# Optimization experiments

Hardware: AMD Instinct MI355X
Metric: run time of the kernel (lower is better)

Reference implementation:

```python
import jax, jax.numpy as jnp
import numpy as np

N_NODES = 50000
N_EDGES = 800000
HIDDEN = 128


def setup_inputs() -> dict:
    key = jax.random.key(0)
    ks = jax.random.split(key, 8)
    z = jax.random.normal(ks[0], (N_NODES, HIDDEN), dtype=jnp.float32)
    weights = jax.random.normal(ks[1], (N_EDGES, 1), dtype=jnp.float32)
    sources = jax.random.randint(ks[2], (N_EDGES,), 0, N_NODES)
    dests = jax.random.randint(ks[3], (N_EDGES,), 0, N_NODES)
    # Linear params (stored [in, out]); scale ~ 1/sqrt(fan_in) like torch default
    in_m = 2 * HIDDEN + 1
    in_u = 2 * HIDDEN
    Wm = jax.random.uniform(ks[4], (in_m, HIDDEN), dtype=jnp.float32, minval=-1.0, maxval=1.0) / np.sqrt(in_m)
    bm = jax.random.uniform(ks[5], (HIDDEN,), dtype=jnp.float32, minval=-1.0, maxval=1.0) / np.sqrt(in_m)
    Wu = jax.random.uniform(ks[6], (in_u, HIDDEN), dtype=jnp.float32, minval=-1.0, maxval=1.0) / np.sqrt(in_u)
    bu = jax.random.uniform(ks[7], (HIDDEN,), dtype=jnp.float32, minval=-1.0, maxval=1.0) / np.sqrt(in_u)
    return {"z": z, "weights": weights, "sources": sources, "dests": dests,
            "Wm": Wm, "bm": bm, "Wu": Wu, "bu": bu}


def reference(z, weights, sources, dests, Wm, bm, Wu, bu):
    n = z.shape[0]
    # gather + concat message input: [E, 2d+1]
    inp = jnp.concatenate([z[dests], z[sources], weights], axis=1)
    messages = inp @ Wm + bm                      # [E, d]
    # scatter_reduce amax over destination nodes; empty segments -> -inf
    m = jax.ops.segment_max(messages, dests, num_segments=n)
    m = jnp.where(jnp.isneginf(m), jnp.zeros_like(m), m)
    h = jnp.concatenate([z, m], axis=1) @ Wu + bu  # [N, d]
    return h
```

## Files before the change

kernel.cpp:

```cpp
#include <hip/hip_runtime.h>
#include <math.h>

#define HIDDEN 128
#define PAD_DEG 64
#define NPART 8
#define CHUNK 2048

typedef __attribute__((ext_vector_type(8))) _Float16 f16x8;
typedef __attribute__((ext_vector_type(4))) float f32x4;
typedef __attribute__((ext_vector_type(2))) _Float16 h2;

__device__ inline unsigned short f2h(float x) {
    _Float16 h = (_Float16)x;
    return __builtin_bit_cast(unsigned short, h);
}
__device__ inline float h2f(unsigned short u) {
    return (float)__builtin_bit_cast(_Float16, u);
}
__device__ inline float h2f_lo(unsigned int u) { return h2f((unsigned short)(u & 0xffff)); }
__device__ inline float h2f_hi(unsigned int u) { return h2f((unsigned short)(u >> 16)); }
__device__ inline h2 hmax2(h2 a, h2 b) {
    h2 r;
    r[0] = a[0] > b[0] ? a[0] : b[0];
    r[1] = a[1] > b[1] ? a[1] : b[1];
    return r;
}

__global__ void prep_kernel(const float* __restrict__ Wm, const float* __restrict__ Wu,
                            unsigned short* __restrict__ WmT0, unsigned short* __restrict__ WmT1,
                            unsigned short* __restrict__ WuT, float* __restrict__ wlast,
                            int* __restrict__ counts, int n) {
    int t = blockIdx.x * blockDim.x + threadIdx.x;
    if (t < 16384) {
        int nn = t >> 7, k = t & 127;
        WmT0[t] = f2h(Wm[k * 128 + nn]);
    } else if (t < 32768) {
        int s = t - 16384;
        int nn = s >> 7, k = s & 127;
        WmT1[s] = f2h(Wm[(128 + k) * 128 + nn]);
    } else if (t < 65536) {
        int s = t - 32768;
        int nn = s >> 8, k = s & 255;
        WuT[s] = f2h(Wu[k * 128 + nn]);
    } else if (t < 65664) {
        int i = t - 65536;
        wlast[i] = Wm[256 * 128 + i];
    } else if (t < 65664 + n) {
        counts[t - 65664] = 0;
    }
}

__global__ __launch_bounds__(256) void gemm_msg(const float* __restrict__ Z,
                                                const unsigned short* __restrict__ WmT0,
                                                const unsigned short* __restrict__ WmT1,
                                                unsigned short* __restrict__ P1h,
                                                unsigned short* __restrict__ P2h,
                                                int n) {
    __shared__ unsigned short As[64][136];
    __shared__ unsigned short Bs[128][136];

    const int m0 = blockIdx.x * 64;
    const int tid = threadIdx.x;
    const int wave = tid >> 6, lane = tid & 63;
    const int l15 = lane & 15, q = lane >> 4;
    const int wrow = wave * 16;

#pragma unroll
    for (int i = 0; i < 4; ++i) {
        int f = tid + i * 256;
        int row = f >> 4, c8 = f & 15;
        int gr = min(m0 + row, n - 1);
        const float4* src = (const float4*)&Z[(size_t)gr * 128 + c8 * 8];
        float4 a = src[0], b = src[1];
        f16x8 hv;
        hv[0] = (_Float16)a.x; hv[1] = (_Float16)a.y; hv[2] = (_Float16)a.z; hv[3] = (_Float16)a.w;
        hv[4] = (_Float16)b.x; hv[5] = (_Float16)b.y; hv[6] = (_Float16)b.z; hv[7] = (_Float16)b.w;
        *(f16x8*)&As[row][c8 * 8] = hv;
    }

    for (int part = 0; part < 2; ++part) {
        const float4* bsrc = (const float4*)(part == 0 ? WmT0 : WmT1);
        unsigned short* Out = part == 0 ? P1h : P2h;

#pragma unroll
        for (int i = 0; i < 8; ++i) {
            int f = tid + i * 256;
            int row = f >> 4, c4 = f & 15;
            *(float4*)&Bs[row][c4 * 8] = bsrc[row * 16 + c4];
        }
        __syncthreads();

        f32x4 acc[8];
#pragma unroll
        for (int nt = 0; nt < 8; ++nt) acc[nt] = (f32x4){0.f, 0.f, 0.f, 0.f};

#pragma unroll
        for (int ks = 0; ks < 4; ++ks) {
            int k0 = ks * 32;
            f16x8 a = *(const f16x8*)&As[wrow + l15][k0 + q * 8];
#pragma unroll
            for (int nt = 0; nt < 8; ++nt) {
                f16x8 b = *(const f16x8*)&Bs[nt * 16 + l15][k0 + q * 8];
                acc[nt] = __builtin_amdgcn_mfma_f32_16x16x32_f16(a, b, acc[nt], 0, 0, 0);
            }
        }

#pragma unroll
        for (int nt = 0; nt < 8; ++nt) {
#pragma unroll
            for (int r = 0; r < 4; ++r) {
                int row = m0 + wrow + q * 4 + r;
                if (row < n) Out[(size_t)row * 128 + nt * 16 + l15] = f2h(acc[nt][r]);
            }
        }
        __syncthreads();
    }
}

__global__ __launch_bounds__(256) void scatter_part(const int* __restrict__ dests,
                                                    const int* __restrict__ sources,
                                                    const float* __restrict__ weights,
                                                    int* __restrict__ counts,
                                                    unsigned int* __restrict__ edge_pk,
                                                    int E, int span, int n) {
    const int part = blockIdx.x & (NPART - 1);
    const int chunk = blockIdx.x >> 3;
    const int lo = part * span;
    const int hi = min(lo + span, n);
    const int base = chunk * CHUNK;

#pragma unroll
    for (int i = 0; i < CHUNK; i += 256) {
        int e = base + i + threadIdx.x;
        if (e < E) {
            int d = dests[e];
            if (d >= lo && d < hi) {
                int pos = atomicAdd(&counts[d], 1);
                if (pos < PAD_DEG) {
                    unsigned int pk = (unsigned int)(sources[e] & 0xffff) |
                                      ((unsigned int)f2h(weights[e]) << 16);
                    edge_pk[(size_t)d * PAD_DEG + pos] = pk;
                }
            }
        }
    }
}

__global__ __launch_bounds__(256) void segmax_kernel(const unsigned short* __restrict__ P1h,
                                                     const unsigned short* __restrict__ P2h,
                                                     const int* __restrict__ counts,
                                                     const unsigned int* __restrict__ edge_pk,
                                                     const float* __restrict__ wlast,
                                                     const float* __restrict__ bm,
                                                     unsigned short* __restrict__ Mh, int n) {
    const int wave = threadIdx.x >> 6;
    const int lane = threadIdx.x & 63;
    const int v = blockIdx.x * 4 + wave;
    if (v >= n) return;

    const int l32 = lane & 31;
    const int half = lane >> 5;
    const uint2* P2q = (const uint2*)P2h;
    const int cnt = min(counts[v], PAD_DEG);

    int pk = (lane < cnt) ? (int)edge_pk[(size_t)v * PAD_DEG + lane] : 0;

    float4 wl4 = ((const float4*)wlast)[l32];
    h2 wlv0; wlv0[0] = (_Float16)wl4.x; wlv0[1] = (_Float16)wl4.y;
    h2 wlv1; wlv1[0] = (_Float16)wl4.z; wlv1[1] = (_Float16)wl4.w;

    const h2 NEGINF = __builtin_bit_cast(h2, 0xFC00FC00u);
    h2 acc0 = NEGINF, acc1 = NEGINF;

    int j = 0;
    for (; j + 4 <= cnt; j += 4) {
        unsigned int pa = (unsigned int)__shfl(pk, j + half);
        unsigned int pb = (unsigned int)__shfl(pk, j + 2 + half);
        {
            int src = pa & 0xffff;
            unsigned int wd = (pa & 0xffff0000u) | (pa >> 16);
            h2 wv = __builtin_bit_cast(h2, wd);
            uint2 u = P2q[(size_t)src * 32 + l32];
            acc0 = hmax2(acc0, wv * wlv0 + __builtin_bit_cast(h2, u.x));
            acc1 = hmax2(acc1, wv * wlv1 + __builtin_bit_cast(h2, u.y));
        }
        {
            int src = pb & 0xffff;
            unsigned int wd = (pb & 0xffff0000u) | (pb >> 16);
            h2 wv = __builtin_bit_cast(h2, wd);
            uint2 u = P2q[(size_t)src * 32 + l32];
            acc0 = hmax2(acc0, wv * wlv0 + __builtin_bit_cast(h2, u.x));
            acc1 = hmax2(acc1, wv * wlv1 + __builtin_bit_cast(h2, u.y));
        }
    }
    for (; j + 2 <= cnt; j += 2) {
        unsigned int pa = (unsigned int)__shfl(pk, j + half);
        int src = pa & 0xffff;
        unsigned int wd = (pa & 0xffff0000u) | (pa >> 16);
        h2 wv = __builtin_bit_cast(h2, wd);
        uint2 u = P2q[(size_t)src * 32 + l32];
        acc0 = hmax2(acc0, wv * wlv0 + __builtin_bit_cast(h2, u.x));
        acc1 = hmax2(acc1, wv * wlv1 + __builtin_bit_cast(h2, u.y));
    }
    if (j < cnt) {
        unsigned int pa = (unsigned int)__shfl(pk, j);
        if (half == 0) {
            int src = pa & 0xffff;
            unsigned int wd = (pa & 0xffff0000u) | (pa >> 16);
            h2 wv = __builtin_bit_cast(h2, wd);
            uint2 u = P2q[(size_t)src * 32 + l32];
            acc0 = hmax2(acc0, wv * wlv0 + __builtin_bit_cast(h2, u.x));
            acc1 = hmax2(acc1, wv * wlv1 + __builtin_bit_cast(h2, u.y));
        }
    }

    acc0 = hmax2(acc0, __builtin_bit_cast(h2, __shfl_xor(__builtin_bit_cast(int, acc0), 32)));
    acc1 = hmax2(acc1, __builtin_bit_cast(h2, __shfl_xor(__builtin_bit_cast(int, acc1), 32)));

    if (half == 0) {
        float m0 = 0.f, m1 = 0.f, m2 = 0.f, m3 = 0.f;
        if (cnt > 0) {
            uint2 p1v = ((const uint2*)P1h)[(size_t)v * 32 + l32];
            float4 b4 = ((const float4*)bm)[l32];
            m0 = h2f_lo(p1v.x) + b4.x + (float)acc0[0];
            m1 = h2f_hi(p1v.x) + b4.y + (float)acc0[1];
            m2 = h2f_lo(p1v.y) + b4.z + (float)acc1[0];
            m3 = h2f_hi(p1v.y) + b4.w + (float)acc1[1];
        }
        uint2 o;
        o.x = (unsigned int)f2h(m0) | ((unsigned int)f2h(m1) << 16);
        o.y = (unsigned int)f2h(m2) | ((unsigned int)f2h(m3) << 16);
        ((uint2*)Mh)[(size_t)v * 32 + l32] = o;
    }
}

__global__ __launch_bounds__(256) void gemm_out(const float* __restrict__ Z,
                                                const unsigned short* __restrict__ Mh,
                                                const unsigned short* __restrict__ WuT,
                                                const float* __restrict__ bu,
                                                float* __restrict__ H, int n) {
    __shared__ unsigned short As[64][136];
    __shared__ unsigned short Bs[128][136];

    const int m0 = blockIdx.x * 64;
    const int tid = threadIdx.x;
    const int wave = tid >> 6, lane = tid & 63;
    const int l15 = lane & 15, q = lane >> 4;
    const int wrow = wave * 16;

    f32x4 acc[8];
#pragma unroll
    for (int nt = 0; nt < 8; ++nt) acc[nt] = (f32x4){0.f, 0.f, 0.f, 0.f};

    for (int h = 0; h < 2; ++h) {
#pragma unroll
        for (int i = 0; i < 8; ++i) {
            int f = tid + i * 256;
            int row = f >> 4, c4 = f & 15;
            *(float4*)&Bs[row][c4 * 8] = ((const float4*)WuT)[row * 32 + h * 16 + c4];
        }
        if (h == 0) {
#pragma unroll
            for (int i = 0; i < 4; ++i) {
                int f = tid + i * 256;
                int row = f >> 4, c8 = f & 15;
                int gr = min(m0 + row, n - 1);
                const float4* src = (const float4*)&Z[(size_t)gr * 128 + c8 * 8];
                float4 a = src[0], b = src[1];
                f16x8 hv;
                hv[0] = (_Float16)a.x; hv[1] = (_Float16)a.y; hv[2] = (_Float16)a.z; hv[3] = (_Float16)a.w;
                hv[4] = (_Float16)b.x; hv[5] = (_Float16)b.y; hv[6] = (_Float16)b.z; hv[7] = (_Float16)b.w;
                *(f16x8*)&As[row][c8 * 8] = hv;
            }
        } else {
#pragma unroll
            for (int i = 0; i < 4; ++i) {
                int f = tid + i * 256;
                int row = f >> 4, c4 = f & 15;
                int gr = min(m0 + row, n - 1);
                *(float4*)&As[row][c4 * 8] = ((const float4*)&Mh[(size_t)gr * 128])[c4];
            }
        }
        __syncthreads();

#pragma unroll
        for (int ks = 0; ks < 4; ++ks) {
            int k0 = ks * 32;
            f16x8 a = *(const f16x8*)&As[wrow + l15][k0 + q * 8];
#pragma unroll
            for (int nt = 0; nt < 8; ++nt) {
                f16x8 b = *(const f16x8*)&Bs[nt * 16 + l15][k0 + q * 8];
                acc[nt] = __builtin_amdgcn_mfma_f32_16x16x32_f16(a, b, acc[nt], 0, 0, 0);
            }
        }
        __syncthreads();
    }

#pragma unroll
    for (int nt = 0; nt < 8; ++nt) {
        int col = nt * 16 + l15;
        float bias = bu[col];
#pragma unroll
        for (int r = 0; r < 4; ++r) {
            int row = m0 + wrow + q * 4 + r;
            if (row < n) H[(size_t)row * 128 + col] = acc[nt][r] + bias;
        }
    }
}

extern "C" void kernel_launch(void* const* d_in, const int* in_sizes, int n_in,
                              void* d_out, int out_size, void* d_ws, size_t ws_size,
                              hipStream_t stream) {
    const float* z = (const float*)d_in[0];
    const float* weights = (const float*)d_in[1];
    const int* sources = (const int*)d_in[2];
    const int* dests = (const int*)d_in[3];
    const float* Wm = (const float*)d_in[4];
    const float* bm = (const float*)d_in[5];
    const float* Wu = (const float*)d_in[6];
    const float* bu = (const float*)d_in[7];

    const int n = in_sizes[0] / HIDDEN;
    const int E = in_sizes[1];
    float* H = (float*)d_out;

    char* w = (char*)d_ws;
    auto alloc = [&](size_t bytes) { void* p = w; w += (bytes + 255) & ~(size_t)255; return p; };
    unsigned short* P1h = (unsigned short*)alloc((size_t)n * 128 * 2);
    unsigned short* Mh  = (unsigned short*)alloc((size_t)n * 128 * 2);
    unsigned short* WmT0 = (unsigned short*)alloc(16384 * 2);
    unsigned short* WmT1 = (unsigned short*)alloc(16384 * 2);
    unsigned short* WuT  = (unsigned short*)alloc(32768 * 2);
    float* wlast = (float*)alloc(128 * 4);
    int* counts  = (int*)alloc((size_t)n * 4);
    unsigned int* edge_pk = (unsigned int*)alloc((size_t)n * PAD_DEG * 4);

    unsigned short* P2h = (unsigned short*)d_out;

    const int mblocks = (n + 63) / 64;
    const int prep_threads = 65664 + n;
    const int span = (n + NPART - 1) / NPART;
    const int nchunks = (E + CHUNK - 1) / CHUNK;

    prep_kernel<<<(prep_threads + 255) / 256, 256, 0, stream>>>(Wm, Wu, WmT0, WmT1, WuT,
                                                                wlast, counts, n);
    gemm_msg<<<mblocks, 256, 0, stream>>>(z, WmT0, WmT1, P1h, P2h, n);
    scatter_part<<<nchunks * NPART, 256, 0, stream>>>(dests, sources, weights, counts,
                                                      edge_pk, E, span, n);
    segmax_kernel<<<(n + 3) / 4, 256, 0, stream>>>(P1h, P2h, counts, edge_pk,
                                                   wlast, bm, Mh, n);
    gemm_out<<<mblocks, 256, 0, stream>>>(z, Mh, WuT, bu, H, n);
}
```

Before: 192.7 us.

## Replace partition-filtered edge scatter with two-pass binning through staging buckets

The old scatter kernel read every edge once per destination partition (8 passes) and filtered by range. Now a binning kernel reads each edge once and uses wave ballots with one atomic per wave per partition to append packed (dest, source|weight) entries into 64 staging buckets. A placement kernel, with blocks interleaved by partition, then does the per-node atomic slot assignment into the padded adjacency. This trades the repeated edge reads for an extra launch and a staging write and read-back. Buckets are capped at a fixed capacity, so skewed destination distributions could silently drop edges.

```diff
diff --git a/kernel.cpp b/kernel.cpp
--- a/kernel.cpp
+++ b/kernel.cpp
@@ -5,6 +5,8 @@
 #define PAD_DEG 64
 #define NPART 8
 #define CHUNK 2048
+#define CAP 16384
+#define PB_J 48
 
 typedef __attribute__((ext_vector_type(8))) _Float16 f16x8;
 typedef __attribute__((ext_vector_type(4))) float f32x4;
@@ -29,7 +31,7 @@
 __global__ void prep_kernel(const float* __restrict__ Wm, const float* __restrict__ Wu,
                             unsigned short* __restrict__ WmT0, unsigned short* __restrict__ WmT1,
                             unsigned short* __restrict__ WuT, float* __restrict__ wlast,
-                            int* __restrict__ counts, int n) {
+                            int* __restrict__ counts, int* __restrict__ pcur, int n) {
     int t = blockIdx.x * blockDim.x + threadIdx.x;
     if (t < 16384) {
         int nn = t >> 7, k = t & 127;
@@ -47,6 +49,8 @@
         wlast[i] = Wm[256 * 128 + i];
     } else if (t < 65664 + n) {
         counts[t - 65664] = 0;
+    } else if (t < 65664 + n + 64) {
+        pcur[t - 65664 - n] = 0;
     }
 }
 
@@ -117,31 +121,62 @@
     }
 }
 
-__global__ __launch_bounds__(256) void scatter_part(const int* __restrict__ dests,
-                                                    const int* __restrict__ sources,
-                                                    const float* __restrict__ weights,
-                                                    int* __restrict__ counts,
-                                                    unsigned int* __restrict__ edge_pk,
-                                                    int E, int span, int n) {
-    const int part = blockIdx.x & (NPART - 1);
-    const int chunk = blockIdx.x >> 3;
-    const int lo = part * span;
-    const int hi = min(lo + span, n);
-    const int base = chunk * CHUNK;
+__global__ __launch_bounds__(256) void bin_kernel(const int* __restrict__ dests,
+                                                  const int* __restrict__ sources,
+                                                  const float* __restrict__ weights,
+                                                  int* __restrict__ pcur,
+                                                  uint2* __restrict__ staging,
+                                                  int E, int span) {
+    const int myb = blockIdx.x & 7;
+    const int base = blockIdx.x * CHUNK;
+    const int lane = threadIdx.x & 63;
 
 #pragma unroll
     for (int i = 0; i < CHUNK; i += 256) {
         int e = base + i + threadIdx.x;
-        if (e < E) {
-            int d = dests[e];
-            if (d >= lo && d < hi) {
-                int pos = atomicAdd(&counts[d], 1);
-                if (pos < PAD_DEG) {
-                    unsigned int pk = (unsigned int)(sources[e] & 0xffff) |
-                                      ((unsigned int)f2h(weights[e]) << 16);
-                    edge_pk[(size_t)d * PAD_DEG + pos] = pk;
-                }
-            }
+        bool valid = e < E;
+        int d = 0;
+        unsigned int pk = 0;
+        if (valid) {
+            d = dests[e];
+            pk = (unsigned int)(sources[e] & 0xffff) |
+                 ((unsigned int)f2h(weights[e]) << 16);
+        }
+        int p = valid ? (d / span) : -1;
+#pragma unroll
+        for (int pp = 0; pp < NPART; ++pp) {
+            unsigned long long m = __ballot(p == pp);
+            if (m == 0ull) continue;
+            int leader = __ffsll((long long)m) - 1;
+            int cnt = __popcll(m);
+            int rbase = 0;
+            if (lane == leader) rbase = atomicAdd(&pcur[pp * 8 + myb], cnt);
+            rbase = __shfl(rbase, leader);
+            if (p == pp) {
+                int off = __popcll(m & ((1ull << lane) - 1ull));
+                int idx = rbase + off;
+                if (idx < CAP)
+                    staging[(size_t)(pp * 8 + myb) * CAP + idx] = make_uint2((unsigned)d, pk);
+            }
+        }
+    }
+}
+
+__global__ __launch_bounds__(256) void place_kernel(const int* __restrict__ pcur,
+                                                    const uint2* __restrict__ staging,
+                                                    int* __restrict__ counts,
+                                                    unsigned int* __restrict__ edge_pk) {
+    const int p = blockIdx.x & 7;
+    const int j = blockIdx.x >> 3;
+
+    for (int r = 0; r < 8; ++r) {
+        int total = min(pcur[p * 8 + r], CAP);
+        const uint2* reg = staging + (size_t)(p * 8 + r) * CAP;
+        for (int i = j * 256 + threadIdx.x; i < total; i += PB_J * 256) {
+            uint2 ent = reg[i];
+            int d = (int)ent.x;
+            int pos = atomicAdd(&counts[d], 1);
+            if (pos < PAD_DEG) edge_pk[(size_t)d * PAD_DEG + pos] = ent.y;
         }
     }
 }
@@ -333,20 +368,22 @@
     unsigned short* WuT  = (unsigned short*)alloc(32768 * 2);
     float* wlast = (float*)alloc(128 * 4);
     int* counts  = (int*)alloc((size_t)n * 4);
+    int* pcur    = (int*)alloc(64 * 4);
     unsigned int* edge_pk = (unsigned int*)alloc((size_t)n * PAD_DEG * 4);
+    uint2* staging = (uint2*)alloc((size_t)64 * CAP * 8);
 
     unsigned short* P2h = (unsigned short*)d_out;
 
     const int mblocks = (n + 63) / 64;
-    const int prep_threads = 65664 + n;
+    const int prep_threads = 65664 + n + 64;
     const int span = (n + NPART - 1) / NPART;
     const int nchunks = (E + CHUNK - 1) / CHUNK;
 
     prep_kernel<<<(prep_threads + 255) / 256, 256, 0, stream>>>(Wm, Wu, WmT0, WmT1, WuT,
-                                                                wlast, counts, n);
+                                                                wlast, counts, pcur, n);
     gemm_msg<<<mblocks, 256, 0, stream>>>(z, WmT0, WmT1, P1h, P2h, n);
-    scatter_part<<<nchunks * NPART, 256, 0, stream>>>(dests, sources, weights, counts,
-                                                      edge_pk, E, span, n);
+    bin_kernel<<<nchunks, 256, 0, stream>>>(dests, sources, weights, pcur, staging, E, span);
+    place_kernel<<<NPART * PB_J, 256, 0, stream>>>(pcur, staging, counts, edge_pk);
     segmax_kernel<<<(n + 3) / 4, 256, 0, stream>>>(P1h, P2h, counts, edge_pk,
                                                    wlast, bm, Mh, n);
     gemm_out<<<mblocks, 256, 0, stream>>>(z, Mh, WuT, bu, H, n);
```

Result: slower. 707.5 us (+267.1%).

## Fuse message GEMM with edge scatter and drop LDS staging in GEMMs

Applied to the files above, without the earlier changes.

Merges the message GEMM and the edge-bucketing scatter into one launch: the first blocks do the GEMM and the remaining blocks do the scatter. This removes one launch and lets the compute-bound and atomic-bound work overlap on the GPU. Both GEMM kernels also stop staging A and B tiles in shared memory and stop calling __syncthreads. Each lane now loads its MFMA fragments straight from global memory (Z, Mh and the transposed weights), relying on cache hits for the reused weight tiles. The risk is more global and L2 traffic, and less coalesced fragment loads, in exchange for no LDS use and no barriers.

```diff
diff --git a/kernel.cpp b/kernel.cpp
--- a/kernel.cpp
+++ b/kernel.cpp
@@ -50,96 +50,81 @@
     }
 }
 
-__global__ __launch_bounds__(256) void gemm_msg(const float* __restrict__ Z,
-                                                const unsigned short* __restrict__ WmT0,
-                                                const unsigned short* __restrict__ WmT1,
-                                                unsigned short* __restrict__ P1h,
-                                                unsigned short* __restrict__ P2h,
-                                                int n) {
-    __shared__ unsigned short As[64][136];
-    __shared__ unsigned short Bs[128][136];
-
-    const int m0 = blockIdx.x * 64;
+__global__ __launch_bounds__(256) void fused_msg_scatter(
+        const float* __restrict__ Z,
+        const unsigned short* __restrict__ WmT0,
+        const unsigned short* __restrict__ WmT1,
+        unsigned short* __restrict__ P1h,
+        unsigned short* __restrict__ P2h,
+        const int* __restrict__ dests,
+        const int* __restrict__ sources,
+        const float* __restrict__ weights,
+        int* __restrict__ counts,
+        unsigned int* __restrict__ edge_pk,
+        int n, int E, int span, int mblocks) {
     const int tid = threadIdx.x;
-    const int wave = tid >> 6, lane = tid & 63;
-    const int l15 = lane & 15, q = lane >> 4;
-    const int wrow = wave * 16;
-
-#pragma unroll
-    for (int i = 0; i < 4; ++i) {
-        int f = tid + i * 256;
-        int row = f >> 4, c8 = f & 15;
-        int gr = min(m0 + row, n - 1);
-        const float4* src = (const float4*)&Z[(size_t)gr * 128 + c8 * 8];
-        float4 a = src[0], b = src[1];
-        f16x8 hv;
-        hv[0] = (_Float16)a.x; hv[1] = (_Float16)a.y; hv[2] = (_Float16)a.z; hv[3] = (_Float16)a.w;
-        hv[4] = (_Float16)b.x; hv[5] = (_Float16)b.y; hv[6] = (_Float16)b.z; hv[7] = (_Float16)b.w;
-        *(f16x8*)&As[row][c8 * 8] = hv;
-    }
-
-    for (int part = 0; part < 2; ++part) {
-        const float4* bsrc = (const float4*)(part == 0 ? WmT0 : WmT1);
-        unsigned short* Out = part == 0 ? P1h : P2h;
-
-#pragma unroll
-        for (int i = 0; i < 8; ++i) {
-            int f = tid + i * 256;
-            int row = f >> 4, c4 = f & 15;
-            *(float4*)&Bs[row][c4 * 8] = bsrc[row * 16 + c4];
-        }
-        __syncthreads();
-
-        f32x4 acc[8];
-#pragma unroll
-        for (int nt = 0; nt < 8; ++nt) acc[nt] = (f32x4){0.f, 0.f, 0.f, 0.f};
-
-#pragma unroll
-        for (int ks = 0; ks < 4; ++ks) {
-            int k0 = ks * 32;
-            f16x8 a = *(const f16x8*)&As[wrow + l15][k0 + q * 8];
+
+    if ((int)blockIdx.x < mblocks) {
+        const int m0 = blockIdx.x * 64;
+        const int wave = tid >> 6, lane = tid & 63;
+        const int l15 = lane & 15, q = lane >> 4;
+        const int row_a = min(m0 + wave * 16 + l15, n - 1);
+
+#pragma unroll
+        for (int part = 0; part < 2; ++part) {
+            const unsigned short* BT = part == 0 ? WmT0 : WmT1;
+            unsigned short* Out = part == 0 ? P1h : P2h;
+
+            f32x4 acc[8];
+#pragma unroll
+            for (int nt = 0; nt < 8; ++nt) acc[nt] = (f32x4){0.f, 0.f, 0.f, 0.f};
+
+#pragma unroll
+            for (int ks = 0; ks < 4; ++ks) {
+                int k0 = ks * 32;
+                const float4* zp = (const float4*)&Z[(size_t)row_a * 128 + k0 + q * 8];
+                float4 z0 = zp[0], z1 = zp[1];
+                f16x8 a;
+                a[0] = (_Float16)z0.x; a[1] = (_Float16)z0.y;
+                a[2] = (_Float16)z0.z; a[3] = (_Float16)z0.w;
+                a[4] = (_Float16)z1.x; a[5] = (_Float16)z1.y;
+                a[6] = (_Float16)z1.z; a[7] = (_Float16)z1.w;
+#pragma unroll
+                for (int nt = 0; nt < 8; ++nt) {
+                    f16x8 b = *(const f16x8*)&BT[(size_t)(nt * 16 + l15) * 128 + k0 + q * 8];
+                    acc[nt] = __builtin_amdgcn_mfma_f32_16x16x32_f16(a, b, acc[nt], 0, 0, 0);
+                }
+            }
+
 #pragma unroll
             for (int nt = 0; nt < 8; ++nt) {
-                f16x8 b = *(const f16x8*)&Bs[nt * 16 + l15][k0 + q * 8];
-                acc[nt] = __builtin_amdgcn_mfma_f32_16x16x32_f16(a, b, acc[nt], 0, 0, 0);
-            }
-        }
-
-#pragma unroll
-        for (int nt = 0; nt < 8; ++nt) {
-#pragma unroll
-            for (int r = 0; r < 4; ++r) {
-                int row = m0 + wrow + q * 4 + r;
-                if (row < n) Out[(size_t)row * 128 + nt * 16 + l15] = f2h(acc[nt][r]);
-            }
-        }
-        __syncthreads();
-    }
-}
-
-__global__ __launch_bounds__(256) void scatter_part(const int* __restrict__ dests,
-                                                    const int* __restrict__ sources,
-                                                    const float* __restrict__ weights,
-                                                    int* __restrict__ counts,
-                                                    unsigned int* __restrict__ edge_pk,
-                                                    int E, int span, int n) {
-    const int part = blockIdx.x & (NPART - 1);
-    const int chunk = blockIdx.x >> 3;
-    const int lo = part * span;
-    const int hi = min(lo + span, n);
-    const int base = chunk * CHUNK;
-
-#pragma unroll
-    for (int i = 0; i < CHUNK; i += 256) {
-        int e = base + i + threadIdx.x;
-        if (e < E) {
-            int d = dests[e];
-            if (d >= lo && d < hi) {
-                int pos = atomicAdd(&counts[d], 1);
-                if (pos < PAD_DEG) {
-                    unsigned int pk = (unsigned int)(sources[e] & 0xffff) |
-                                      ((unsigned int)f2h(weights[e]) << 16);
-                    edge_pk[(size_t)d * PAD_DEG + pos] = pk;
+#pragma unroll
+                for (int r = 0; r < 4; ++r) {
+                    int row = m0 + wave * 16 + q * 4 + r;
+                    if (row < n) Out[(size_t)row * 128 + nt * 16 + l15] = f2h(acc[nt][r]);
+                }
+            }
+        }
+    } else {
+        const int sblk = blockIdx.x - mblocks;
+        const int part = blockIdx.x & (NPART - 1);
+        const int chunk = sblk >> 3;
+        const int lo = part * span;
+        const int hi = min(lo + span, n);
+        const int base = chunk * CHUNK;
+
+#pragma unroll
+        for (int i = 0; i < CHUNK; i += 256) {
+            int e = base + i + tid;
+            if (e < E) {
+                int d = dests[e];
+                if (d >= lo && d < hi) {
+                    int pos = atomicAdd(&counts[d], 1);
+                    if (pos < PAD_DEG) {
+                        unsigned int pk = (unsigned int)(sources[e] & 0xffff) |
+                                          ((unsigned int)f2h(weights[e]) << 16);
+                        edge_pk[(size_t)d * PAD_DEG + pos] = pk;
+                    }
                 }
             }
         }
@@ -239,61 +224,38 @@
                                                 const unsigned short* __restrict__ WuT,
                                                 const float* __restrict__ bu,
                                                 float* __restrict__ H, int n) {
-    __shared__ unsigned short As[64][136];
-    __shared__ unsigned short Bs[128][136];
-
     const int m0 = blockIdx.x * 64;
     const int tid = threadIdx.x;
     const int wave = tid >> 6, lane = tid & 63;
     const int l15 = lane & 15, q = lane >> 4;
-    const int wrow = wave * 16;
+    const int row_a = min(m0 + wave * 16 + l15, n - 1);
 
     f32x4 acc[8];
 #pragma unroll
     for (int nt = 0; nt < 8; ++nt) acc[nt] = (f32x4){0.f, 0.f, 0.f, 0.f};
 
+#pragma unroll
     for (int h = 0; h < 2; ++h) {
-#pragma unroll
-        for (int i = 0; i < 8; ++i) {
-            int f = tid + i * 256;
-            int row = f >> 4, c4 = f & 15;
-            *(float4*)&Bs[row][c4 * 8] = ((const float4*)WuT)[row * 32 + h * 16 + c4];
-        }
-        if (h == 0) {
-#pragma unroll
-            for (int i = 0; i < 4; ++i) {
-                int f = tid + i * 256;
-                int row = f >> 4, c8 = f & 15;
-                int gr = min(m0 + row, n - 1);
-                const float4* src = (const float4*)&Z[(size_t)gr * 128 + c8 * 8];
-                float4 a = src[0], b = src[1];
-                f16x8 hv;
-                hv[0] = (_Float16)a.x; hv[1] = (_Float16)a.y; hv[2] = (_Float16)a.z; hv[3] = (_Float16)a.w;
-                hv[4] = (_Float16)b.x; hv[5] = (_Float16)b.y; hv[6] = (_Float16)b.z; hv[7] = (_Float16)b.w;
-                *(f16x8*)&As[row][c8 * 8] = hv;
-            }
-        } else {
-#pragma unroll
-            for (int i = 0; i < 4; ++i) {
-                int f = tid + i * 256;
-                int row = f >> 4, c4 = f & 15;
-                int gr = min(m0 + row, n - 1);
-                *(float4*)&As[row][c4 * 8] = ((const float4*)&Mh[(size_t)gr * 128])[c4];
-            }
-        }
-        __syncthreads();
-
 #pragma unroll
         for (int ks = 0; ks < 4; ++ks) {
             int k0 = ks * 32;
-            f16x8 a = *(const f16x8*)&As[wrow + l15][k0 + q * 8];
+            f16x8 a;
+            if (h == 0) {
+                const float4* zp = (const float4*)&Z[(size_t)row_a * 128 + k0 + q * 8];
+                float4 z0 = zp[0], z1 = zp[1];
+                a[0] = (_Float16)z0.x; a[1] = (_Float16)z0.y;
+                a[2] = (_Float16)z0.z; a[3] = (_Float16)z0.w;
+                a[4] = (_Float16)z1.x; a[5] = (_Float16)z1.y;
+                a[6] = (_Float16)z1.z; a[7] = (_Float16)z1.w;
+            } else {
+                a = *(const f16x8*)&Mh[(size_t)row_a * 128 + k0 + q * 8];
+            }
 #pragma unroll
             for (int nt = 0; nt < 8; ++nt) {
-                f16x8 b = *(const f16x8*)&Bs[nt * 16 + l15][k0 + q * 8];
+                f16x8 b = *(const f16x8*)&WuT[(size_t)(nt * 16 + l15) * 256 + h * 128 + k0 + q * 8];
                 acc[nt] = __builtin_amdgcn_mfma_f32_16x16x32_f16(a, b, acc[nt], 0, 0, 0);
             }
         }
-        __syncthreads();
     }
 
 #pragma unroll
@@ -302,7 +264,7 @@
         float bias = bu[col];
 #pragma unroll
         for (int r = 0; r < 4; ++r) {
-            int row = m0 + wrow + q * 4 + r;
+            int row = m0 + wave * 16 + q * 4 + r;
             if (row < n) H[(size_t)row * 128 + col] = acc[nt][r] + bias;
         }
     }
@@ -344,9 +306,9 @@
 
     prep_kernel<<<(prep_threads + 255) / 256, 256, 0, stream>>>(Wm, Wu, WmT0, WmT1, WuT,
                                                                 wlast, counts, n);
-    gemm_msg<<<mblocks, 256, 0, stream>>>(z, WmT0, WmT1, P1h, P2h, n);
-    scatter_part<<<nchunks * NPART, 256, 0, stream>>>(dests, sources, weights, counts,
-                                                      edge_pk, E, span, n);
+    fused_msg_scatter<<<mblocks + nchunks * NPART, 256, 0, stream>>>(
+        z, WmT0, WmT1, P1h, P2h, dests, sources, weights, counts, edge_pk,
+        n, E, span, mblocks);
     segmax_kernel<<<(n + 3) / 4, 256, 0, stream>>>(P1h, P2h, counts, edge_pk,
                                                    wlast, bm, Mh, n);
     gemm_out<<<mblocks, 256, 0, stream>>>(z, Mh, WuT, bu, H, n);
```

Result: slower. 234.7 us (+21.8%).
